# Kernel tuning notes

Measured on AMD Instinct MI355X. Metric: run time of the kernel, lower is better.

## Reference

```python
import jax, jax.numpy as jnp
import numpy as np


def squash(s):
    # v = (|s|^2 / (1 + |s|^2)) * s / |s|, norm over last axis
    sn = jnp.sum(s * s, axis=-1, keepdims=True)
    return sn / (1.0 + sn) * s / jnp.sqrt(sn)


def setup_inputs() -> dict:
    key = jax.random.key(0)
    k1, k2, k3 = jax.random.split(key, 3)
    N, C, D, W, H = 32, 32, 16, 16, 16
    K, P = 10, 4
    l = jax.random.normal(k1, (N, C, D, W, H), dtype=jnp.float32)
    g = jax.random.normal(k2, (N, K, D), dtype=jnp.float32)
    weight = jax.random.normal(k3, (1, C, 1, K, P, P), dtype=jnp.float32)
    return {"l": l, "g": g, "weight": weight, "n_rout": 3}


def reference(l, g, weight, n_rout):
    N, C, D, W, H = l.shape
    K = weight.shape[3]
    P = weight.shape[-1]  # D == P*P
    # (N,C,D,W,H) -> (N,C,W*H,P,P)
    lr = jnp.transpose(l, (0, 1, 3, 4, 2)).reshape(N, C, W * H, P, P)
    # per-capsule 4x4 vote matmul against per-(channel,class) weight
    wt = weight[0, :, 0]  # (C,K,P,P)
    V = jnp.einsum('ncsij,ckjd->ncskid', lr, wt)  # (N,C,S,K,P,P)
    B = C * W * H
    V = V.reshape(N, B, K, P * P)  # (N,B,K,D) votes
    # initial logits from global capsule g: b = <g, V> over D
    b = jnp.sum(g[:, None, :, :] * V, axis=-1, keepdims=True)  # (N,B,K,1)
    gc = None
    for _ in range(n_rout):
        c = jax.nn.softmax(b, axis=2)                 # softmax over classes K
        s = jnp.sum(V * c, axis=1, keepdims=True)     # (N,1,K,D)
        gc = squash(s)                                # (N,1,K,D)
        b = jnp.sum(gc * V, axis=-1, keepdims=True)   # (N,B,K,1)
    a = jax.nn.sigmoid(jnp.sqrt(jnp.sum(gc * gc, axis=-1)))  # (N,1,K)
    return a.reshape(N, K), gc.reshape(N, K, P * P)
```

## Files before the change

kernel.cpp:

```cpp
#include <hip/hip_runtime.h>


#define KK 10
#define PP 16
#define CC 32
#define SS 256
#define NN 32

__global__ __launch_bounds__(256, 4) void iter_kernel(
    const float* __restrict__ l,
    const float* __restrict__ w,
    const float* __restrict__ g,
    const float* __restrict__ s_prev,
    float* __restrict__ s_next,
    const int first)
{
  const int bid = blockIdx.x;
  const int n = bid >> 5;
  const int c = bid & 31;
  const int t = threadIdx.x;

  __shared__ float lr_lds[PP][SS + 4];
  __shared__ float ct[KK][SS + 4];
  __shared__ float U_lds[KK * PP];
  __shared__ float w_lds[KK * PP];
  __shared__ float gc_lds[KK * PP];
  __shared__ float f_lds[KK];
  __shared__ float part[KK][PP][PP + 1];

  if (t < KK * PP) w_lds[t] = w[c * KK * PP + t];
  float lr[PP];
  const float* lb = l + (size_t)(n * CC + c) * (PP * SS) + t;
  #pragma unroll
  for (int d = 0; d < PP; ++d) {
    lr[d] = lb[d * SS];
    lr_lds[d][t] = lr[d];
  }

  if (first) {
    if (t < KK * PP) gc_lds[t] = g[n * KK * PP + t];
    __syncthreads();
  } else {
    if (t < KK * PP) gc_lds[t] = s_prev[n * KK * PP + t];
    __syncthreads();
    if (t < KK) {
      float sn = 0.f;
      #pragma unroll
      for (int m = 0; m < PP; ++m) { const float v = gc_lds[t * PP + m]; sn += v * v; }
      f_lds[t] = sn / (1.f + sn) * rsqrtf(sn);
    }
    __syncthreads();
    if (t < KK * PP) gc_lds[t] *= f_lds[t >> 4];
    __syncthreads();
  }

  if (t < KK * PP) {
    const int k = t >> 4, ij = t & 15, i = ij >> 2, j = ij & 3;
    const float4 wv = *(const float4*)&w_lds[k * PP + j * 4];
    const float4 gv = *(const float4*)&gc_lds[k * PP + i * 4];
    U_lds[t] = wv.x * gv.x + wv.y * gv.y + wv.z * gv.z + wv.w * gv.w;
  }
  __syncthreads();

  {
    float b[KK];
    float bmax = -1e30f;
    #pragma unroll
    for (int k = 0; k < KK; ++k) {
      float acc = 0.f;
      #pragma unroll
      for (int d4 = 0; d4 < 4; ++d4) {
        const float4 uv = *(const float4*)&U_lds[k * PP + d4 * 4];
        acc += lr[d4*4+0]*uv.x + lr[d4*4+1]*uv.y + lr[d4*4+2]*uv.z + lr[d4*4+3]*uv.w;
      }
      b[k] = acc;
      bmax = fmaxf(bmax, acc);
    }
    float ssum = 0.f;
    #pragma unroll
    for (int k = 0; k < KK; ++k) { b[k] = __expf(b[k] - bmax); ssum += b[k]; }
    const float inv = 1.f / ssum;
    #pragma unroll
    for (int k = 0; k < KK; ++k) ct[k][t] = b[k] * inv;
  }
  __syncthreads();

  {
    const int ch = t >> 4;
    const int ij = t & 15;
    const int sbase = ch * 16;
    float acc[KK];
    #pragma unroll
    for (int k = 0; k < KK; ++k) acc[k] = 0.f;
    #pragma unroll
    for (int s4 = 0; s4 < 4; ++s4) {
      const float4 lv = *(const float4*)&lr_lds[ij][sbase + s4 * 4];
      #pragma unroll
      for (int k = 0; k < KK; ++k) {
        const float4 cv = *(const float4*)&ct[k][sbase + s4 * 4];
        acc[k] += cv.x*lv.x + cv.y*lv.y + cv.z*lv.z + cv.w*lv.w;
      }
    }
    #pragma unroll
    for (int k = 0; k < KK; ++k) part[k][ij][ch] = acc[k];
  }
  __syncthreads();

  if (t < KK * PP) {
    const int k = t >> 4, ij = t & 15;
    float m = 0.f;
    #pragma unroll
    for (int s4 = 0; s4 < 4; ++s4) {
      const float4 pv = *(const float4*)&part[k][ij][s4 * 4];
      m += pv.x + pv.y + pv.z + pv.w;
    }
    U_lds[t] = m;
  }
  __syncthreads();

  if (t < KK * PP) {
    const int k = t >> 4, i = (t >> 2) & 3, d = t & 3;
    const float* Mp  = U_lds + k * PP + i * 4;
    const float* wpt = w_lds + k * PP + d;
    const float sv = Mp[0]*wpt[0] + Mp[1]*wpt[4] + Mp[2]*wpt[8] + Mp[3]*wpt[12];
    atomicAdd(&s_next[n * KK * PP + t], sv);
  }
}

__global__ __launch_bounds__(256) void final_kernel(
    const float* __restrict__ s_last,
    float* __restrict__ out_a,
    float* __restrict__ out_gc)
{
  const int n = blockIdx.x;
  const int t = threadIdx.x;
  __shared__ float s_lds[KK * PP];
  __shared__ float f_lds[KK];
  if (t < KK * PP) s_lds[t] = s_last[n * KK * PP + t];
  __syncthreads();
  if (t < KK) {
    float sn = 0.f;
    #pragma unroll
    for (int m = 0; m < PP; ++m) { const float v = s_lds[t * PP + m]; sn += v * v; }
    f_lds[t] = sn / (1.f + sn) * rsqrtf(sn);
    const float gn = sn / (1.f + sn);
    out_a[n * KK + t] = 1.f / (1.f + __expf(-gn));
  }
  __syncthreads();
  if (t < KK * PP) out_gc[n * KK * PP + t] = s_lds[t] * f_lds[t >> 4];
}

extern "C" void kernel_launch(void* const* d_in, const int* in_sizes, int n_in,
                              void* d_out, int out_size, void* d_ws, size_t ws_size,
                              hipStream_t stream) {
  const float* l = (const float*)d_in[0];
  const float* g = (const float*)d_in[1];
  const float* w = (const float*)d_in[2];

  float* out    = (float*)d_out;
  float* out_a  = out;
  float* out_gc = out + NN * KK;

  float* s_buf = (float*)d_ws;
  const size_t s_bytes = (size_t)3 * NN * KK * PP * sizeof(float);
  hipMemsetAsync(s_buf, 0, s_bytes, stream);

  float* s0 = s_buf;
  float* s1 = s_buf + NN * KK * PP;
  float* s2 = s_buf + 2 * NN * KK * PP;

  iter_kernel<<<NN * CC, 256, 0, stream>>>(l, w, g, (const float*)nullptr, s0, 1);
  iter_kernel<<<NN * CC, 256, 0, stream>>>(l, w, g, s0, s1, 0);
  iter_kernel<<<NN * CC, 256, 0, stream>>>(l, w, g, s1, s2, 0);
  final_kernel<<<NN, 256, 0, stream>>>(s2, out_a, out_gc);
}
```

Measured before the change: 89.09 us.

## Fuse routing iterations into one persistent kernel with per-sample atomic barriers

Replaces the three iteration launches and the final launch with a single kernel in which 1024-thread blocks handle four channels of one sample. Each block keeps its slice of l in registers and LDS across iterations, and uses atomic counters to spin-wait until all 8 blocks of a sample have contributed before reading the reduced s. This is meant to remove launch overhead and repeated global loads of l. It relies on all 256 blocks being co-resident, otherwise the spin-waits can deadlock (bounded by a guard). It also adds a cross-wave shuffle reduction step.

```diff
diff --git a/kernel.cpp b/kernel.cpp
--- a/kernel.cpp
+++ b/kernel.cpp
@@ -6,148 +6,185 @@
 #define CC 32
 #define SS 256
 #define NN 32
-
-__global__ __launch_bounds__(256, 4) void iter_kernel(
+#define RR 3
+#define GR 4
+#define BPN 8
+
+__global__ __launch_bounds__(1024, 4) void fused_kernel(
     const float* __restrict__ l,
     const float* __restrict__ w,
     const float* __restrict__ g,
-    const float* __restrict__ s_prev,
-    float* __restrict__ s_next,
-    const int first)
+    float* __restrict__ s_buf,
+    int*   __restrict__ ctr,
+    float* __restrict__ out_a,
+    float* __restrict__ out_gc)
 {
   const int bid = blockIdx.x;
-  const int n = bid >> 5;
-  const int c = bid & 31;
-  const int t = threadIdx.x;
-
-  __shared__ float lr_lds[PP][SS + 4];
-  __shared__ float ct[KK][SS + 4];
-  __shared__ float U_lds[KK * PP];
-  __shared__ float w_lds[KK * PP];
+  const int n   = bid >> 3;
+  const int cg  = bid & 7;
+  const int t   = threadIdx.x;
+  const int grp = t >> 8;
+  const int tt  = t & 255;
+  const int c   = cg * GR + grp;
+
+  __shared__ float lr_lds[GR][PP][SS + 4];
+  __shared__ float ct_lds[GR][KK][SS + 4];
+  __shared__ float w_lds[GR][KK * PP];
+  __shared__ float U_lds[GR][KK * PP];
+  __shared__ float pmerge[GR][4][KK * PP];
+  __shared__ float sred[GR][KK * PP];
   __shared__ float gc_lds[KK * PP];
   __shared__ float f_lds[KK];
-  __shared__ float part[KK][PP][PP + 1];
-
-  if (t < KK * PP) w_lds[t] = w[c * KK * PP + t];
+
+  if (tt < KK * PP) w_lds[grp][tt] = w[c * KK * PP + tt];
   float lr[PP];
-  const float* lb = l + (size_t)(n * CC + c) * (PP * SS) + t;
+  const float* lb = l + (size_t)(n * CC + c) * (PP * SS) + tt;
   #pragma unroll
   for (int d = 0; d < PP; ++d) {
     lr[d] = lb[d * SS];
-    lr_lds[d][t] = lr[d];
+    lr_lds[grp][d][tt] = lr[d];
   }
-
-  if (first) {
-    if (t < KK * PP) gc_lds[t] = g[n * KK * PP + t];
-    __syncthreads();
-  } else {
-    if (t < KK * PP) gc_lds[t] = s_prev[n * KK * PP + t];
+  if (t < KK * PP) gc_lds[t] = g[n * KK * PP + t];
+  __syncthreads();
+
+  #pragma unroll 1
+  for (int r = 0; r < RR; ++r) {
+    if (r > 0) {
+      if (t < KK) {
+        float sn = 0.f;
+        #pragma unroll
+        for (int m = 0; m < PP; ++m) { const float v = gc_lds[t * PP + m]; sn += v * v; }
+        f_lds[t] = sn / (1.f + sn) * rsqrtf(sn);
+      }
+      __syncthreads();
+      if (t < KK * PP) gc_lds[t] *= f_lds[t >> 4];
+      __syncthreads();
+    }
+
+    if (tt < KK * PP) {
+      const int k = tt >> 4, ij = tt & 15, i = ij >> 2, j = ij & 3;
+      const float4 wv = *(const float4*)&w_lds[grp][k * PP + j * 4];
+      const float4 gv = *(const float4*)&gc_lds[k * PP + i * 4];
+      U_lds[grp][tt] = wv.x * gv.x + wv.y * gv.y + wv.z * gv.z + wv.w * gv.w;
+    }
+    __syncthreads();
+
+    {
+      float b[KK];
+      float bmax = -1e30f;
+      #pragma unroll
+      for (int k = 0; k < KK; ++k) {
+        float acc = 0.f;
+        #pragma unroll
+        for (int d4 = 0; d4 < 4; ++d4) {
+          const float4 uv = *(const float4*)&U_lds[grp][k * PP + d4 * 4];
+          acc += lr[d4*4+0]*uv.x + lr[d4*4+1]*uv.y + lr[d4*4+2]*uv.z + lr[d4*4+3]*uv.w;
+        }
+        b[k] = acc;
+        bmax = fmaxf(bmax, acc);
+      }
+      float ssum = 0.f;
+      #pragma unroll
+      for (int k = 0; k < KK; ++k) { b[k] = __expf(b[k] - bmax); ssum += b[k]; }
+      const float inv = 1.f / ssum;
+      #pragma unroll
+      for (int k = 0; k < KK; ++k) ct_lds[grp][k][tt] = b[k] * inv;
+    }
+    __syncthreads();
+
+    {
+      const int ch = tt >> 4, ij = tt & 15, sbase = ch * 16;
+      float acc[KK];
+      #pragma unroll
+      for (int k = 0; k < KK; ++k) acc[k] = 0.f;
+      #pragma unroll
+      for (int s4 = 0; s4 < 4; ++s4) {
+        const float4 lv = *(const float4*)&lr_lds[grp][ij][sbase + s4 * 4];
+        #pragma unroll
+        for (int k = 0; k < KK; ++k) {
+          const float4 cv = *(const float4*)&ct_lds[grp][k][sbase + s4 * 4];
+          acc[k] += cv.x*lv.x + cv.y*lv.y + cv.z*lv.z + cv.w*lv.w;
+        }
+      }
+      #pragma unroll
+      for (int k = 0; k < KK; ++k) {
+        acc[k] += __shfl_xor(acc[k], 16);
+        acc[k] += __shfl_xor(acc[k], 32);
+      }
+      const int wv = tt >> 6;
+      if ((tt & 63) < 16) {
+        #pragma unroll
+        for (int k = 0; k < KK; ++k) pmerge[grp][wv][k * PP + ij] = acc[k];
+      }
+    }
+    __syncthreads();
+
+    if (tt < KK * PP) {
+      U_lds[grp][tt] = pmerge[grp][0][tt] + pmerge[grp][1][tt]
+                     + pmerge[grp][2][tt] + pmerge[grp][3][tt];
+    }
+    __syncthreads();
+
+    if (tt < KK * PP) {
+      const int k = tt >> 4, i = (tt >> 2) & 3, d = tt & 3;
+      const float* Mp  = &U_lds[grp][k * PP + i * 4];
+      const float* wpt = &w_lds[grp][k * PP + d];
+      sred[grp][tt] = Mp[0]*wpt[0] + Mp[1]*wpt[4] + Mp[2]*wpt[8] + Mp[3]*wpt[12];
+    }
+    __syncthreads();
+
+    float* s_r = s_buf + (size_t)r * NN * KK * PP;
+    if (t < KK * PP) {
+      atomicAdd(&s_r[n * KK * PP + t],
+                sred[0][t] + sred[1][t] + sred[2][t] + sred[3][t]);
+    }
+    __syncthreads();
+
+    if (t == 0)
+      __hip_atomic_fetch_add(&ctr[r * NN + n], 1,
+                             __ATOMIC_RELEASE, __HIP_MEMORY_SCOPE_AGENT);
+
+    if (r < RR - 1) {
+      if (t == 0) {
+        int guard = 0;
+        while (__hip_atomic_load(&ctr[r * NN + n],
+                                 __ATOMIC_RELAXED, __HIP_MEMORY_SCOPE_AGENT) < BPN
+               && ++guard < (1 << 24))
+          __builtin_amdgcn_s_sleep(2);
+      }
+      __syncthreads();
+      if (t < KK * PP)
+        gc_lds[t] = __hip_atomic_load(&s_r[n * KK * PP + t],
+                                      __ATOMIC_RELAXED, __HIP_MEMORY_SCOPE_AGENT);
+      __syncthreads();
+    }
+  }
+
+  if (cg == 0) {
+    float* s2 = s_buf + (size_t)2 * NN * KK * PP;
+    if (t == 0) {
+      int guard = 0;
+      while (__hip_atomic_load(&ctr[2 * NN + n],
+                               __ATOMIC_RELAXED, __HIP_MEMORY_SCOPE_AGENT) < BPN
+             && ++guard < (1 << 24))
+        __builtin_amdgcn_s_sleep(2);
+    }
+    __syncthreads();
+    if (t < KK * PP)
+      gc_lds[t] = __hip_atomic_load(&s2[n * KK * PP + t],
+                                    __ATOMIC_RELAXED, __HIP_MEMORY_SCOPE_AGENT);
     __syncthreads();
     if (t < KK) {
       float sn = 0.f;
       #pragma unroll
       for (int m = 0; m < PP; ++m) { const float v = gc_lds[t * PP + m]; sn += v * v; }
       f_lds[t] = sn / (1.f + sn) * rsqrtf(sn);
-    }
-    __syncthreads();
-    if (t < KK * PP) gc_lds[t] *= f_lds[t >> 4];
-    __syncthreads();
+      const float gn = sn / (1.f + sn);
+      out_a[n * KK + t] = 1.f / (1.f + __expf(-gn));
+    }
+    __syncthreads();
+    if (t < KK * PP) out_gc[n * KK * PP + t] = gc_lds[t] * f_lds[t >> 4];
   }
-
-  if (t < KK * PP) {
-    const int k = t >> 4, ij = t & 15, i = ij >> 2, j = ij & 3;
-    const float4 wv = *(const float4*)&w_lds[k * PP + j * 4];
-    const float4 gv = *(const float4*)&gc_lds[k * PP + i * 4];
-    U_lds[t] = wv.x * gv.x + wv.y * gv.y + wv.z * gv.z + wv.w * gv.w;
-  }
-  __syncthreads();
-
-  {
-    float b[KK];
-    float bmax = -1e30f;
-    #pragma unroll
-    for (int k = 0; k < KK; ++k) {
-      float acc = 0.f;
-      #pragma unroll
-      for (int d4 = 0; d4 < 4; ++d4) {
-        const float4 uv = *(const float4*)&U_lds[k * PP + d4 * 4];
-        acc += lr[d4*4+0]*uv.x + lr[d4*4+1]*uv.y + lr[d4*4+2]*uv.z + lr[d4*4+3]*uv.w;
-      }
-      b[k] = acc;
-      bmax = fmaxf(bmax, acc);
-    }
-    float ssum = 0.f;
-    #pragma unroll
-    for (int k = 0; k < KK; ++k) { b[k] = __expf(b[k] - bmax); ssum += b[k]; }
-    const float inv = 1.f / ssum;
-    #pragma unroll
-    for (int k = 0; k < KK; ++k) ct[k][t] = b[k] * inv;
-  }
-  __syncthreads();
-
-  {
-    const int ch = t >> 4;
-    const int ij = t & 15;
-    const int sbase = ch * 16;
-    float acc[KK];
-    #pragma unroll
-    for (int k = 0; k < KK; ++k) acc[k] = 0.f;
-    #pragma unroll
-    for (int s4 = 0; s4 < 4; ++s4) {
-      const float4 lv = *(const float4*)&lr_lds[ij][sbase + s4 * 4];
-      #pragma unroll
-      for (int k = 0; k < KK; ++k) {
-        const float4 cv = *(const float4*)&ct[k][sbase + s4 * 4];
-        acc[k] += cv.x*lv.x + cv.y*lv.y + cv.z*lv.z + cv.w*lv.w;
-      }
-    }
-    #pragma unroll
-    for (int k = 0; k < KK; ++k) part[k][ij][ch] = acc[k];
-  }
-  __syncthreads();
-
-  if (t < KK * PP) {
-    const int k = t >> 4, ij = t & 15;
-    float m = 0.f;
-    #pragma unroll
-    for (int s4 = 0; s4 < 4; ++s4) {
-      const float4 pv = *(const float4*)&part[k][ij][s4 * 4];
-      m += pv.x + pv.y + pv.z + pv.w;
-    }
-    U_lds[t] = m;
-  }
-  __syncthreads();
-
-  if (t < KK * PP) {
-    const int k = t >> 4, i = (t >> 2) & 3, d = t & 3;
-    const float* Mp  = U_lds + k * PP + i * 4;
-    const float* wpt = w_lds + k * PP + d;
-    const float sv = Mp[0]*wpt[0] + Mp[1]*wpt[4] + Mp[2]*wpt[8] + Mp[3]*wpt[12];
-    atomicAdd(&s_next[n * KK * PP + t], sv);
-  }
-}
-
-__global__ __launch_bounds__(256) void final_kernel(
-    const float* __restrict__ s_last,
-    float* __restrict__ out_a,
-    float* __restrict__ out_gc)
-{
-  const int n = blockIdx.x;
-  const int t = threadIdx.x;
-  __shared__ float s_lds[KK * PP];
-  __shared__ float f_lds[KK];
-  if (t < KK * PP) s_lds[t] = s_last[n * KK * PP + t];
-  __syncthreads();
-  if (t < KK) {
-    float sn = 0.f;
-    #pragma unroll
-    for (int m = 0; m < PP; ++m) { const float v = s_lds[t * PP + m]; sn += v * v; }
-    f_lds[t] = sn / (1.f + sn) * rsqrtf(sn);
-    const float gn = sn / (1.f + sn);
-    out_a[n * KK + t] = 1.f / (1.f + __expf(-gn));
-  }
-  __syncthreads();
-  if (t < KK * PP) out_gc[n * KK * PP + t] = s_lds[t] * f_lds[t >> 4];
 }
 
 extern "C" void kernel_launch(void* const* d_in, const int* in_sizes, int n_in,
@@ -162,15 +199,12 @@
   float* out_gc = out + NN * KK;
 
   float* s_buf = (float*)d_ws;
-  const size_t s_bytes = (size_t)3 * NN * KK * PP * sizeof(float);
-  hipMemsetAsync(s_buf, 0, s_bytes, stream);
-
-  float* s0 = s_buf;
-  float* s1 = s_buf + NN * KK * PP;
-  float* s2 = s_buf + 2 * NN * KK * PP;
-
-  iter_kernel<<<NN * CC, 256, 0, stream>>>(l, w, g, (const float*)nullptr, s0, 1);
-  iter_kernel<<<NN * CC, 256, 0, stream>>>(l, w, g, s0, s1, 0);
-  iter_kernel<<<NN * CC, 256, 0, stream>>>(l, w, g, s1, s2, 0);
-  final_kernel<<<NN, 256, 0, stream>>>(s2, out_a, out_gc);
+  int*   ctr   = (int*)((char*)d_ws +
+                        (size_t)3 * NN * KK * PP * sizeof(float));
+  const size_t zero_bytes =
+      (size_t)3 * NN * KK * PP * sizeof(float) + (size_t)3 * NN * sizeof(int);
+  hipMemsetAsync(d_ws, 0, zero_bytes, stream);
+
+  fused_kernel<<<NN * BPN, 1024, 0, stream>>>(l, w, g, s_buf, ctr,
+                                              out_a, out_gc);
 }
```

After: 101.0 us. 13.4% more time.
